# Performance work log

Hardware: AMD Instinct MI355X
Metric: run time of the kernel (lower is better)

## Reference

```python
import jax, jax.numpy as jnp
import numpy as np

D_MODEL, EXPAND, D_STATE, D_CONV, HEADDIM = 1024, 2, 64, 4, 64
D_INNER = EXPAND * D_MODEL          # 2048
NHEADS = D_INNER // HEADDIM         # 32
CONV_DIM = D_INNER + 2 * D_STATE    # x, B, C go through the depthwise conv
D_IN_PROJ = 2 * D_INNER + 2 * D_STATE + NHEADS  # z, xBC, dt
EPS = 1e-5


def setup_inputs() -> dict:
    key = jax.random.key(0)
    ks = jax.random.split(key, 16)
    s = 0.02
    inp = {
        "x": jax.random.normal(ks[0], (2, 2048, D_MODEL), jnp.float32),
        "ln1_w": jnp.ones((D_MODEL,), jnp.float32),
        "ln1_b": jnp.zeros((D_MODEL,), jnp.float32),
        "in_proj_w": jax.random.normal(ks[1], (D_IN_PROJ, D_MODEL), jnp.float32) * s,
        "conv_w": jax.random.normal(ks[2], (CONV_DIM, D_CONV), jnp.float32) * 0.3,
        "conv_b": jnp.zeros((CONV_DIM,), jnp.float32),
        # dt_bias so that softplus(dt+dt_bias) lands in ~[1e-3, 0.1] (mamba2 init)
        "dt_bias": jnp.log(jnp.expm1(jnp.exp(jax.random.uniform(ks[3], (NHEADS,), jnp.float32, jnp.log(1e-3), jnp.log(0.1))))),
        "A_log": jnp.log(jax.random.uniform(ks[4], (NHEADS,), jnp.float32, 1.0, 16.0)),
        "D": jnp.ones((NHEADS,), jnp.float32),
        "norm_w": jnp.ones((D_INNER,), jnp.float32),
        "out_proj_w": jax.random.normal(ks[5], (D_MODEL, D_INNER), jnp.float32) * s,
        "ln2_w": jnp.ones((D_MODEL,), jnp.float32),
        "ln2_b": jnp.zeros((D_MODEL,), jnp.float32),
        "mlp_w1": jax.random.normal(ks[6], (4 * D_MODEL, D_MODEL), jnp.float32) * s,
        "mlp_b1": jnp.zeros((4 * D_MODEL,), jnp.float32),
        "mlp_w2": jax.random.normal(ks[7], (D_MODEL, 4 * D_MODEL), jnp.float32) * s,
        "mlp_b2": jnp.zeros((D_MODEL,), jnp.float32),
    }
    return inp


def _layernorm(x, w, b):
    mu = jnp.mean(x, axis=-1, keepdims=True)
    var = jnp.mean(jnp.square(x - mu), axis=-1, keepdims=True)
    return (x - mu) * jax.lax.rsqrt(var + EPS) * w + b


def _mamba2(x, in_proj_w, conv_w, conv_b, dt_bias, A_log, D, norm_w, out_proj_w):
    Bt, L, _ = x.shape
    zxbcdt = x @ in_proj_w.T                                  # [B,L,D_IN_PROJ]
    z = zxbcdt[..., :D_INNER]
    xBC = zxbcdt[..., D_INNER:D_INNER + CONV_DIM]
    dt = jax.nn.softplus(zxbcdt[..., D_INNER + CONV_DIM:] + dt_bias)  # [B,L,H]
    # causal depthwise conv1d, kernel D_CONV, then SiLU
    xp = jnp.pad(xBC, ((0, 0), (D_CONV - 1, 0), (0, 0)))
    conv = conv_b
    for k in range(D_CONV):
        conv = conv + xp[:, k:k + L, :] * conv_w[:, k]
    xBC = jax.nn.silu(conv)
    xs = xBC[..., :D_INNER].reshape(Bt, L, NHEADS, HEADDIM)   # [B,L,H,P]
    Bm = xBC[..., D_INNER:D_INNER + D_STATE]                  # [B,L,N] (ngroups=1)
    Cm = xBC[..., D_INNER + D_STATE:]                         # [B,L,N]
    A = -jnp.exp(A_log)                                       # [H]

    def step(h, inp):
        x_t, dt_t, B_t, C_t = inp                             # [B,H,P],[B,H],[B,N],[B,N]
        dA = jnp.exp(dt_t * A)                                # [B,H]
        h = h * dA[:, :, None, None] + (dt_t[:, :, None] * x_t)[..., None] * B_t[:, None, None, :]
        y = jnp.einsum('bhpn,bn->bhp', h, C_t)
        return h, y

    h0 = jnp.zeros((Bt, NHEADS, HEADDIM, D_STATE), x.dtype)
    xsT = jnp.moveaxis(xs, 1, 0)
    dtT = jnp.moveaxis(dt, 1, 0)
    BT = jnp.moveaxis(Bm, 1, 0)
    CT = jnp.moveaxis(Cm, 1, 0)
    _, ys = jax.lax.scan(step, h0, (xsT, dtT, BT, CT))        # ys: [L,B,H,P]
    y = jnp.moveaxis(ys, 0, 1) + xs * D[None, None, :, None]  # skip D
    y = y.reshape(Bt, L, D_INNER)
    # gated RMSNorm: rmsnorm(y * silu(z)) * norm_w
    y = y * jax.nn.silu(z)
    y = y * jax.lax.rsqrt(jnp.mean(jnp.square(y), axis=-1, keepdims=True) + EPS) * norm_w
    return y @ out_proj_w.T


def reference(x, ln1_w, ln1_b, in_proj_w, conv_w, conv_b, dt_bias, A_log, D,
              norm_w, out_proj_w, ln2_w, ln2_b, mlp_w1, mlp_b1, mlp_w2, mlp_b2):
    res = x
    h = _layernorm(x, ln1_w, ln1_b)
    h = _mamba2(h, in_proj_w, conv_w, conv_b, dt_bias, A_log, D, norm_w, out_proj_w)
    x = res + h
    res = x
    h = _layernorm(x, ln2_w, ln2_b)
    h = jax.nn.gelu(h @ mlp_w1.T + mlp_b1, approximate=False) @ mlp_w2.T + mlp_b2
    return res + h
```

## Files before the change

kernel.cpp:

```cpp
#include <hip/hip_runtime.h>
#include <hip/hip_bf16.h>
#include <math.h>

using bf16 = __hip_bfloat16;
typedef __attribute__((ext_vector_type(8))) short short8;
typedef __attribute__((ext_vector_type(4))) float floatx4;

#define SEQLEN   2048
#define ROWS     4096
#define DMODEL   1024
#define DINNER   2048
#define NHEADS   32
#define HEADDIM  64
#define DSTATE   64
#define CONVDIM  2176
#define DINPROJ  4256
#define NCHUNK   32

__device__ __forceinline__ float b2f(bf16 x) { return __bfloat162float(x); }
__device__ __forceinline__ bf16  f2b(float x) { return __float2bfloat16(x); }
__device__ __forceinline__ float s2f(short s) { union { short s; bf16 b; } u; u.s = s; return b2f(u.b); }
__device__ __forceinline__ short f2s(float f) { union { short s; bf16 b; } u; u.b = f2b(f); return u.s; }
__device__ __forceinline__ float tof(float x) { return x; }
__device__ __forceinline__ float tof(bf16 x)  { return __bfloat162float(x); }

typedef __attribute__((address_space(1))) void v_as1;
typedef __attribute__((address_space(3))) void v_as3;
__device__ __forceinline__ void gload_lds16(const void* g, void* l) {
  __builtin_amdgcn_global_load_lds((v_as1*)(g), (v_as3*)(l), 16, 0, 0);
}

__global__ void cvt_kernel(const float* __restrict__ in, bf16* __restrict__ out, int n4) {
  int i = blockIdx.x * 256 + threadIdx.x;
  if (i < n4) {
    float4 v = ((const float4*)in)[i];
    union { bf16 h[4]; uint2 u; } r;
    r.h[0] = f2b(v.x); r.h[1] = f2b(v.y); r.h[2] = f2b(v.z); r.h[3] = f2b(v.w);
    ((uint2*)out)[i] = r.u;
  }
}

__device__ __forceinline__ void block_reduce_2(float& a, float& b) {
#pragma unroll
  for (int off = 32; off > 0; off >>= 1) {
    a += __shfl_xor(a, off);
    b += __shfl_xor(b, off);
  }
  __shared__ float ra[4], rb[4];
  int w = threadIdx.x >> 6;
  if ((threadIdx.x & 63) == 0) { ra[w] = a; rb[w] = b; }
  __syncthreads();
  a = ra[0] + ra[1] + ra[2] + ra[3];
  b = rb[0] + rb[1] + rb[2] + rb[3];
}

template<typename TIN>
__global__ void ln_kernel(const TIN* __restrict__ x, const float* __restrict__ w,
                          const float* __restrict__ b, bf16* __restrict__ out)
{
  int row = blockIdx.x;
  int tid = threadIdx.x;
  float v[4]; float s = 0.f, sq = 0.f;
#pragma unroll
  for (int k = 0; k < 4; ++k) {
    int c = k * 256 + tid;
    float xv = tof(x[(size_t)row * DMODEL + c]);
    v[k] = xv; s += xv; sq += xv * xv;
  }
  block_reduce_2(s, sq);
  float mu  = s * (1.f / DMODEL);
  float var = sq * (1.f / DMODEL) - mu * mu;
  float rs  = rsqrtf(var + 1e-5f);
#pragma unroll
  for (int k = 0; k < 4; ++k) {
    int c = k * 256 + tid;
    out[(size_t)row * DMODEL + c] = f2b((v[k] - mu) * rs * w[c] + b[c]);
  }
}

template<int EPI>
__device__ __forceinline__ void epi_store(float v, size_t off, int col,
                                          const float* bias, const void* resid, void* Cout)
{
  if (EPI == 0) {
    ((bf16*)Cout)[off] = f2b(v);
  } else if (EPI == 1) {
    v += bias[col];
    v = 0.5f * v * (1.f + erff(v * 0.70710678118654752f));
    ((bf16*)Cout)[off] = f2b(v);
  } else if (EPI == 2) {
    v += ((const float*)resid)[off];
    ((bf16*)Cout)[off] = f2b(v);
  } else {
    v += bias[col] + b2f(((const bf16*)resid)[off]);
    ((float*)Cout)[off] = v;
  }
}


template<int EPI>
__global__ __launch_bounds__(256, 2)
void gemm_bt(const bf16* __restrict__ A, const bf16* __restrict__ W,
             const float* __restrict__ bias, const void* __restrict__ resid,
             void* __restrict__ Cout, int M, int N, int K)
{
  __shared__ __align__(16) short Asl[128 * 64];
  __shared__ __align__(16) short Bsl[128 * 64];
  const int tid  = threadIdx.x;
  const int lane = tid & 63;
  const int wv   = tid >> 6;
  const int wm   = wv >> 1, wn = wv & 1;
  const int r16  = lane & 15, q = lane >> 4;
  const int m0   = blockIdx.x * 128;
  const int n0   = blockIdx.y * 128;

  floatx4 acc[4][4] = {};

  for (int k0 = 0; k0 < K; k0 += 64) {
#pragma unroll
    for (int it = 0; it < 4; ++it) {
      int idx = it * 256 + tid;
      int row = m0 + (idx >> 3);
      int cb  = (((idx & 7) ^ ((idx >> 3) & 7)) << 3);
      gload_lds16(A + (size_t)row * K + k0 + cb, &Asl[idx * 8]);
    }
#pragma unroll
    for (int it = 0; it < 4; ++it) {
      int idx = it * 256 + tid;
      int row = n0 + (idx >> 3);
      if (row > N - 1) row = N - 1;
      int cb  = (((idx & 7) ^ ((idx >> 3) & 7)) << 3);
      gload_lds16(W + (size_t)row * K + k0 + cb, &Bsl[idx * 8]);
    }
    __syncthreads();
#pragma unroll
    for (int kk = 0; kk < 64; kk += 32) {
      short8 af[4], bfr[4];
      const int lb = (kk >> 3) + q;
#pragma unroll
      for (int i = 0; i < 4; ++i) {
        int ar = wm * 64 + i * 16 + r16;
        af[i] = *(const short8*)&Asl[ar * 64 + ((lb ^ (ar & 7)) << 3)];
      }
#pragma unroll
      for (int j = 0; j < 4; ++j) {
        int br = wn * 64 + j * 16 + r16;
        bfr[j] = *(const short8*)&Bsl[br * 64 + ((lb ^ (br & 7)) << 3)];
      }
#pragma unroll
      for (int i = 0; i < 4; ++i)
#pragma unroll
        for (int j = 0; j < 4; ++j)
          acc[i][j] = __builtin_amdgcn_mfma_f32_16x16x32_bf16(af[i], bfr[j], acc[i][j], 0, 0, 0);
    }
    __syncthreads();
  }

#pragma unroll
  for (int i = 0; i < 4; ++i)
#pragma unroll
    for (int j = 0; j < 4; ++j)
#pragma unroll
      for (int r = 0; r < 4; ++r) {
        int row = m0 + wm * 64 + i * 16 + q * 4 + r;
        int col = n0 + wn * 64 + j * 16 + r16;
        if (col < N)
          epi_store<EPI>(acc[i][j][r], (size_t)row * N + col, col, bias, resid, Cout);
      }
}

template<int EPI>
__global__ __launch_bounds__(256, 4)
void gemm_bt_6464(const bf16* __restrict__ A, const bf16* __restrict__ W,
                  const float* __restrict__ bias, const void* __restrict__ resid,
                  void* __restrict__ Cout, int M, int N, int K)
{
  __shared__ __align__(16) short Asl[64 * 64];
  __shared__ __align__(16) short Bsl[64 * 64];
  const int tid  = threadIdx.x;
  const int lane = tid & 63;
  const int wv   = tid >> 6;
  const int wm   = wv >> 1, wn = wv & 1;
  const int r16  = lane & 15, q = lane >> 4;
  const int m0   = blockIdx.x * 64;
  const int n0   = blockIdx.y * 64;

  floatx4 acc[2][2] = {};

  for (int k0 = 0; k0 < K; k0 += 64) {
#pragma unroll
    for (int it = 0; it < 2; ++it) {
      int idx = it * 256 + tid;
      int cb  = (((idx & 7) ^ ((idx >> 3) & 7)) << 3);
      gload_lds16(A + (size_t)(m0 + (idx >> 3)) * K + k0 + cb, &Asl[idx * 8]);
    }
#pragma unroll
    for (int it = 0; it < 2; ++it) {
      int idx = it * 256 + tid;
      int cb  = (((idx & 7) ^ ((idx >> 3) & 7)) << 3);
      gload_lds16(W + (size_t)(n0 + (idx >> 3)) * K + k0 + cb, &Bsl[idx * 8]);
    }
    __syncthreads();
#pragma unroll
    for (int kk = 0; kk < 64; kk += 32) {
      short8 af[2], bfr[2];
      const int lb = (kk >> 3) + q;
#pragma unroll
      for (int i = 0; i < 2; ++i) {
        int ar = wm * 32 + i * 16 + r16;
        af[i] = *(const short8*)&Asl[ar * 64 + ((lb ^ (ar & 7)) << 3)];
      }
#pragma unroll
      for (int j = 0; j < 2; ++j) {
        int br = wn * 32 + j * 16 + r16;
        bfr[j] = *(const short8*)&Bsl[br * 64 + ((lb ^ (br & 7)) << 3)];
      }
#pragma unroll
      for (int i = 0; i < 2; ++i)
#pragma unroll
        for (int j = 0; j < 2; ++j)
          acc[i][j] = __builtin_amdgcn_mfma_f32_16x16x32_bf16(af[i], bfr[j], acc[i][j], 0, 0, 0);
    }
    __syncthreads();
  }

#pragma unroll
  for (int i = 0; i < 2; ++i)
#pragma unroll
    for (int j = 0; j < 2; ++j)
#pragma unroll
      for (int r = 0; r < 4; ++r) {
        int row = m0 + wm * 32 + i * 16 + q * 4 + r;
        int col = n0 + wn * 32 + j * 16 + r16;
        epi_store<EPI>(acc[i][j][r], (size_t)row * N + col, col, bias, resid, Cout);
      }
}

__global__ void conv_kernel(const bf16* __restrict__ zx, const float* __restrict__ cw,
                            const float* __restrict__ cb, const float* __restrict__ dtbias,
                            bf16* __restrict__ xbc, bf16* __restrict__ Bb,
                            bf16* __restrict__ Cbb, float* __restrict__ dtb)
{
  int row = blockIdx.x;
  int b = row >> 11, t = row & 2047;
  for (int c = threadIdx.x; c < CONVDIM; c += 256) {
    float acc = cb[c];
#pragma unroll
    for (int k = 0; k < 4; ++k) {
      int tt = t + k - 3;
      if (tt >= 0)
        acc += b2f(zx[((size_t)(b * SEQLEN + tt)) * DINPROJ + DINNER + c]) * cw[c * 4 + k];
    }
    float s = acc / (1.f + __expf(-acc));
    xbc[(size_t)row * CONVDIM + c] = f2b(s);
    if (c >= DINNER) {
      if (c < DINNER + DSTATE) Bb[row * DSTATE + (c - DINNER)] = f2b(s);
      else                     Cbb[row * DSTATE + (c - DINNER - DSTATE)] = f2b(s);
    }
  }
  if (threadIdx.x < NHEADS) {
    int hh = threadIdx.x;
    float raw = b2f(zx[(size_t)row * DINPROJ + DINNER + CONVDIM + hh]) + dtbias[hh];
    float dt = raw > 20.f ? raw : log1pf(__expf(raw));
    dtb[row * NHEADS + hh] = dt;
  }
}

__device__ __forceinline__ float wave_incl_prefix(float a, int lane) {
#pragma unroll
  for (int off = 1; off < 64; off <<= 1) {
    float o = __shfl_up(a, off);
    if (lane >= off) a += o;
  }
  return a;
}

__global__ __launch_bounds__(64)
void chunk_state_kernel(const bf16* __restrict__ xbc, const bf16* __restrict__ Bb,
                        const float* __restrict__ dtb, const float* __restrict__ A_log,
                        float* __restrict__ Sbuf, float* __restrict__ Pbuf)
{
  const int blk = blockIdx.x;
  const int c = blk & 31, h = (blk >> 5) & 31, b = blk >> 10;
  const int bh = b * 32 + h;
  const int lane = threadIdx.x;
  const int row = b * SEQLEN + c * 64 + lane;
  const float Ah = -__expf(A_log[h]);

  float dts = dtb[row * NHEADS + h];
  float E = wave_incl_prefix(dts * Ah, lane);
  float EQ = __shfl(E, 63);
  float w = __expf(EQ - E) * dts;
  if (lane == 63) Pbuf[bh * NCHUNK + c] = __expf(EQ);

  __shared__ __align__(16) short XwT[64 * 72];
  __shared__ __align__(16) short BT[64 * 72];

  const bf16* xrow = xbc + (size_t)row * CONVDIM + h * 64;
  const bf16* brow = Bb + (size_t)row * DSTATE;
#pragma unroll
  for (int i = 0; i < 8; ++i) {
    short8 xv = *(const short8*)(xrow + i * 8);
    short8 bv = *(const short8*)(brow + i * 8);
#pragma unroll
    for (int j = 0; j < 8; ++j) {
      XwT[(i * 8 + j) * 72 + lane] = f2s(w * s2f(xv[j]));
      BT[(i * 8 + j) * 72 + lane]  = bv[j];
    }
  }
  __syncthreads();

  const int r16 = lane & 15, q = lane >> 4;
  floatx4 acc[4][4] = {};
#pragma unroll
  for (int kk = 0; kk < 64; kk += 32) {
    short8 af[4], bfr[4];
#pragma unroll
    for (int i = 0; i < 4; ++i) af[i]  = *(const short8*)&XwT[(i * 16 + r16) * 72 + kk + q * 8];
#pragma unroll
    for (int j = 0; j < 4; ++j) bfr[j] = *(const short8*)&BT[(j * 16 + r16) * 72 + kk + q * 8];
#pragma unroll
    for (int i = 0; i < 4; ++i)
#pragma unroll
      for (int j = 0; j < 4; ++j)
        acc[i][j] = __builtin_amdgcn_mfma_f32_16x16x32_bf16(af[i], bfr[j], acc[i][j], 0, 0, 0);
  }
  float* Sout = Sbuf + (size_t)(bh * NCHUNK + c) * 4096;
#pragma unroll
  for (int i = 0; i < 4; ++i)
#pragma unroll
    for (int j = 0; j < 4; ++j)
#pragma unroll
      for (int r = 0; r < 4; ++r)
        Sout[(i * 16 + q * 4 + r) * 64 + (j * 16 + r16)] = acc[i][j][r];
}

__global__ __launch_bounds__(64)
void combine_kernel(const float* __restrict__ Sbuf, const float* __restrict__ Pbuf,
                    bf16* __restrict__ HinB)
{
  const int bh = blockIdx.x >> 2, slab = blockIdx.x & 3;
  const int base = slab * 1024 + threadIdx.x * 16;
  float h[16];
#pragma unroll
  for (int k = 0; k < 16; ++k) h[k] = 0.f;
  for (int c = 0; c < NCHUNK; ++c) {
    size_t off = (size_t)(bh * NCHUNK + c) * 4096 + base;
    union { short s[16]; uint4 q[2]; } pk;
#pragma unroll
    for (int k = 0; k < 16; ++k) pk.s[k] = f2s(h[k]);
    *(uint4*)(HinB + off)     = pk.q[0];
    *(uint4*)(HinB + off + 8) = pk.q[1];
    float P = Pbuf[bh * NCHUNK + c];
    const float4* S4 = (const float4*)(Sbuf + off);
#pragma unroll
    for (int k = 0; k < 4; ++k) {
      float4 s = S4[k];
      h[k*4+0] = h[k*4+0] * P + s.x;
      h[k*4+1] = h[k*4+1] * P + s.y;
      h[k*4+2] = h[k*4+2] * P + s.z;
      h[k*4+3] = h[k*4+3] * P + s.w;
    }
  }
}

__global__ __launch_bounds__(64)
void y_kernel(const bf16* __restrict__ xbc, const bf16* __restrict__ Bb,
              const bf16* __restrict__ Cbb, const float* __restrict__ dtb,
              const bf16* __restrict__ HinB, const float* __restrict__ A_log,
              const float* __restrict__ Dp, bf16* __restrict__ yout)
{
  const int blk = blockIdx.x;
  const int c = blk & 31, h = (blk >> 5) & 31, b = blk >> 10;
  const int bh = b * 32 + h;
  const int lane = threadIdx.x;
  const int row0 = b * SEQLEN + c * 64;
  const int row = row0 + lane;
  const float Ah = -__expf(A_log[h]);
  const float Dh = Dp[h];

  __shared__ __align__(16) short XdT[64 * 72];
  __shared__ __align__(16) short Msh[64 * 72];
  __shared__ float Esh[64];

  float dts = dtb[row * NHEADS + h];
  float E = wave_incl_prefix(dts * Ah, lane);
  Esh[lane] = E;

  const bf16* xrow = xbc + (size_t)row * CONVDIM + h * 64;
#pragma unroll
  for (int i = 0; i < 8; ++i) {
    short8 xv = *(const short8*)(xrow + i * 8);
#pragma unroll
    for (int j = 0; j < 8; ++j)
      XdT[(i * 8 + j) * 72 + lane] = f2s(dts * s2f(xv[j]));
  }
  __syncthreads();

  const int r16 = lane & 15, q = lane >> 4;

  floatx4 accg[4][4] = {};
#pragma unroll
  for (int kk = 0; kk < 64; kk += 32) {
    short8 af[4], bfr[4];
#pragma unroll
    for (int i = 0; i < 4; ++i)
      af[i]  = *(const short8*)(Cbb + (size_t)(row0 + i * 16 + r16) * DSTATE + kk + q * 8);
#pragma unroll
    for (int j = 0; j < 4; ++j)
      bfr[j] = *(const short8*)(Bb + (size_t)(row0 + j * 16 + r16) * DSTATE + kk + q * 8);
#pragma unroll
    for (int i = 0; i < 4; ++i)
#pragma unroll
      for (int j = 0; j < 4; ++j)
        accg[i][j] = __builtin_amdgcn_mfma_f32_16x16x32_bf16(af[i], bfr[j], accg[i][j], 0, 0, 0);
  }
#pragma unroll
  for (int i = 0; i < 4; ++i)
#pragma unroll
    for (int j = 0; j < 4; ++j)
#pragma unroll
      for (int r = 0; r < 4; ++r) {
        int t = i * 16 + q * 4 + r;
        int s = j * 16 + r16;
        float v = (s <= t) ? __expf(Esh[t] - Esh[s]) * accg[i][j][r] : 0.f;
        Msh[t * 72 + s] = f2s(v);
      }
  __syncthreads();

  floatx4 acc[4][4] = {};
#pragma unroll
  for (int kk = 0; kk < 64; kk += 32) {
    short8 af[4], bfr[4];
#pragma unroll
    for (int i = 0; i < 4; ++i) af[i]  = *(const short8*)&Msh[(i * 16 + r16) * 72 + kk + q * 8];
#pragma unroll
    for (int j = 0; j < 4; ++j) bfr[j] = *(const short8*)&XdT[(j * 16 + r16) * 72 + kk + q * 8];
#pragma unroll
    for (int i = 0; i < 4; ++i)
#pragma unroll
      for (int j = 0; j < 4; ++j)
        acc[i][j] = __builtin_amdgcn_mfma_f32_16x16x32_bf16(af[i], bfr[j], acc[i][j], 0, 0, 0);
  }
  float ei[4];
#pragma unroll
  for (int i = 0; i < 4; ++i) ei[i] = __expf(Esh[i * 16 + r16]);
  const bf16* hinp = HinB + (size_t)(bh * NCHUNK + c) * 4096;
#pragma unroll
  for (int kk = 0; kk < 64; kk += 32) {
    short8 af[4], bfr[4];
#pragma unroll
    for (int i = 0; i < 4; ++i) {
      short8 cv = *(const short8*)(Cbb + (size_t)(row0 + i * 16 + r16) * DSTATE + kk + q * 8);
#pragma unroll
      for (int jj = 0; jj < 8; ++jj) af[i][jj] = f2s(ei[i] * s2f(cv[jj]));
    }
#pragma unroll
    for (int j = 0; j < 4; ++j)
      bfr[j] = *(const short8*)(hinp + (j * 16 + r16) * 64 + kk + q * 8);
#pragma unroll
    for (int i = 0; i < 4; ++i)
#pragma unroll
      for (int j = 0; j < 4; ++j)
        acc[i][j] = __builtin_amdgcn_mfma_f32_16x16x32_bf16(af[i], bfr[j], acc[i][j], 0, 0, 0);
  }
#pragma unroll
  for (int i = 0; i < 4; ++i)
#pragma unroll
    for (int j = 0; j < 4; ++j)
#pragma unroll
      for (int r = 0; r < 4; ++r) {
        int t = i * 16 + q * 4 + r;
        int p = j * 16 + r16;
        int g = row0 + t;
        float y = acc[i][j][r] + Dh * b2f(xbc[(size_t)g * CONVDIM + h * 64 + p]);
        yout[(size_t)g * DINNER + h * 64 + p] = f2b(y);
      }
}

__global__ void gate_rms_kernel(const bf16* __restrict__ y, const bf16* __restrict__ zx,
                                const float* __restrict__ nw, bf16* __restrict__ yn)
{
  int row = blockIdx.x, tid = threadIdx.x;
  float v[8]; float ss = 0.f, dummy = 0.f;
#pragma unroll
  for (int k = 0; k < 8; ++k) {
    int c = k * 256 + tid;
    float z = b2f(zx[(size_t)row * DINPROJ + c]);
    float g = z / (1.f + __expf(-z));
    float val = b2f(y[(size_t)row * DINNER + c]) * g;
    v[k] = val; ss += val * val;
  }
  block_reduce_2(ss, dummy);
  float rs = rsqrtf(ss * (1.f / DINNER) + 1e-5f);
#pragma unroll
  for (int k = 0; k < 8; ++k) {
    int c = k * 256 + tid;
    yn[(size_t)row * DINNER + c] = f2b(v[k] * rs * nw[c]);
  }
}

extern "C" void kernel_launch(void* const* d_in, const int* in_sizes, int n_in,
                              void* d_out, int out_size, void* d_ws, size_t ws_size,
                              hipStream_t stream)
{
  const float* x         = (const float*)d_in[0];
  const float* ln1_w     = (const float*)d_in[1];
  const float* ln1_b     = (const float*)d_in[2];
  const float* in_proj_w = (const float*)d_in[3];
  const float* conv_w    = (const float*)d_in[4];
  const float* conv_b    = (const float*)d_in[5];
  const float* dt_bias   = (const float*)d_in[6];
  const float* A_log     = (const float*)d_in[7];
  const float* Dp        = (const float*)d_in[8];
  const float* norm_w    = (const float*)d_in[9];
  const float* out_proj_w= (const float*)d_in[10];
  const float* ln2_w     = (const float*)d_in[11];
  const float* ln2_b     = (const float*)d_in[12];
  const float* mlp_w1    = (const float*)d_in[13];
  const float* mlp_b1    = (const float*)d_in[14];
  const float* mlp_w2    = (const float*)d_in[15];
  const float* mlp_b2    = (const float*)d_in[16];

  char* ws = (char*)d_ws;
  bf16*  zx   = (bf16*)(ws + 0);
  bf16*  h1   = (bf16*)(ws + 34865152);
  bf16*  xbc  = (bf16*)(ws + 43253760);
  bf16*  Bb   = (bf16*)(ws + 61079552);
  bf16*  Cbb  = (bf16*)(ws + 61603840);
  float* dtb  = (float*)(ws + 62128128);
  float* Pbuf = (float*)(ws + 62652416);
  float* Sbuf = (float*)(ws + 62660608);
  bf16*  yw   = (bf16*)(ws + 62660608);
  bf16*  x2   = (bf16*)(ws + 79437824);
  bf16*  HinB = (bf16*)(ws + 96215040);
  bf16*  yn   = (bf16*)(ws + 96215040);
  bf16*  wip  = (bf16*)(ws + 112992256);
  bf16*  wop  = (bf16*)(ws + 121708544);
  bf16*  h2n  = h1;
  bf16*  mid  = zx;
  bf16*  w1b  = wip;
  bf16*  w2b  = xbc;

  cvt_kernel<<<(4256 * 1024 / 4 + 255) / 256, 256, 0, stream>>>(in_proj_w, wip, 4256 * 1024 / 4);
  ln_kernel<float><<<ROWS, 256, 0, stream>>>(x, ln1_w, ln1_b, h1);
  gemm_bt<0><<<dim3(32, 34), 256, 0, stream>>>(h1, wip, nullptr, nullptr, zx,
                                               ROWS, DINPROJ, DMODEL);
  cvt_kernel<<<(4096 * 1024 / 4 + 255) / 256, 256, 0, stream>>>(mlp_w1, w1b, 4096 * 1024 / 4);
  cvt_kernel<<<(1024 * 2048 / 4 + 255) / 256, 256, 0, stream>>>(out_proj_w, wop, 1024 * 2048 / 4);
  conv_kernel<<<ROWS, 256, 0, stream>>>(zx, conv_w, conv_b, dt_bias, xbc, Bb, Cbb, dtb);
  chunk_state_kernel<<<2048, 64, 0, stream>>>(xbc, Bb, dtb, A_log, Sbuf, Pbuf);
  combine_kernel<<<256, 64, 0, stream>>>(Sbuf, Pbuf, HinB);
  y_kernel<<<2048, 64, 0, stream>>>(xbc, Bb, Cbb, dtb, HinB, A_log, Dp, yw);
  cvt_kernel<<<(1024 * 4096 / 4 + 255) / 256, 256, 0, stream>>>(mlp_w2, w2b, 1024 * 4096 / 4);
  gate_rms_kernel<<<ROWS, 256, 0, stream>>>(yw, zx, norm_w, yn);
  gemm_bt_6464<2><<<dim3(64, 16), 256, 0, stream>>>(yn, wop, nullptr, x, (void*)x2,
                                                    ROWS, DMODEL, DINNER);
  ln_kernel<bf16><<<ROWS, 256, 0, stream>>>(x2, ln2_w, ln2_b, h2n);
  gemm_bt<1><<<dim3(32, 32), 256, 0, stream>>>(h2n, w1b, mlp_b1, nullptr, mid,
                                               ROWS, 4 * DMODEL, DMODEL);
  gemm_bt_6464<3><<<dim3(64, 16), 256, 0, stream>>>(mid, w2b, mlp_b2, x2, d_out,
                                                    ROWS, DMODEL, 4 * DMODEL);
}
```

Baseline: 430.3 us.

## Use intra-block split-K across waves for 64x64 output-projection and MLP-down GEMMs

The 64x64 tile GEMM now loads 128-wide K slabs, and each of the four waves computes the full 64x64 tile over its own 32-wide K slice instead of a 32x32 sub-tile. Partial sums are reduced through shared memory before the epilogue. The goal is fewer barriers per unit of K and more MFMA work per fragment load. In exchange it uses more accumulator registers (64 floats per lane), larger shared memory, and an extra reduction pass with several syncs that may reduce occupancy.

```diff
diff --git a/kernel.cpp b/kernel.cpp
--- a/kernel.cpp
+++ b/kernel.cpp
@@ -171,69 +171,110 @@
 
 template<int EPI>
 __global__ __launch_bounds__(256, 4)
-void gemm_bt_6464(const bf16* __restrict__ A, const bf16* __restrict__ W,
+void gemm_bt_64sk(const bf16* __restrict__ A, const bf16* __restrict__ W,
                   const float* __restrict__ bias, const void* __restrict__ resid,
                   void* __restrict__ Cout, int M, int N, int K)
 {
-  __shared__ __align__(16) short Asl[64 * 64];
-  __shared__ __align__(16) short Bsl[64 * 64];
+  __shared__ __align__(16) char smem[2][64 * 66 * 4];
+  short* Asl  = (short*)smem[0];
+  short* Bsl  = (short*)smem[1];
+  float* red0 = (float*)smem[0];
+  float* red1 = (float*)smem[1];
+
   const int tid  = threadIdx.x;
   const int lane = tid & 63;
   const int wv   = tid >> 6;
-  const int wm   = wv >> 1, wn = wv & 1;
   const int r16  = lane & 15, q = lane >> 4;
   const int m0   = blockIdx.x * 64;
   const int n0   = blockIdx.y * 64;
 
-  floatx4 acc[2][2] = {};
-
-  for (int k0 = 0; k0 < K; k0 += 64) {
-#pragma unroll
-    for (int it = 0; it < 2; ++it) {
+  floatx4 acc[4][4] = {};
+
+  for (int k0 = 0; k0 < K; k0 += 128) {
+#pragma unroll
+    for (int it = 0; it < 4; ++it) {
       int idx = it * 256 + tid;
-      int cb  = (((idx & 7) ^ ((idx >> 3) & 7)) << 3);
-      gload_lds16(A + (size_t)(m0 + (idx >> 3)) * K + k0 + cb, &Asl[idx * 8]);
-    }
-#pragma unroll
-    for (int it = 0; it < 2; ++it) {
+      int row = idx >> 4;
+      int cb  = (((idx & 15) ^ (row & 15)) << 3);
+      gload_lds16(A + (size_t)(m0 + row) * K + k0 + cb, &Asl[idx * 8]);
+    }
+#pragma unroll
+    for (int it = 0; it < 4; ++it) {
       int idx = it * 256 + tid;
-      int cb  = (((idx & 7) ^ ((idx >> 3) & 7)) << 3);
-      gload_lds16(W + (size_t)(n0 + (idx >> 3)) * K + k0 + cb, &Bsl[idx * 8]);
+      int row = idx >> 4;
+      int cb  = (((idx & 15) ^ (row & 15)) << 3);
+      gload_lds16(W + (size_t)(n0 + row) * K + k0 + cb, &Bsl[idx * 8]);
     }
     __syncthreads();
-#pragma unroll
-    for (int kk = 0; kk < 64; kk += 32) {
-      short8 af[2], bfr[2];
-      const int lb = (kk >> 3) + q;
-#pragma unroll
-      for (int i = 0; i < 2; ++i) {
-        int ar = wm * 32 + i * 16 + r16;
-        af[i] = *(const short8*)&Asl[ar * 64 + ((lb ^ (ar & 7)) << 3)];
+    {
+      short8 af[4], bfr[4];
+      const int lb = wv * 4 + q;
+#pragma unroll
+      for (int i = 0; i < 4; ++i) {
+        int ar = i * 16 + r16;
+        af[i] = *(const short8*)&Asl[ar * 128 + ((lb ^ (ar & 15)) << 3)];
       }
 #pragma unroll
-      for (int j = 0; j < 2; ++j) {
-        int br = wn * 32 + j * 16 + r16;
-        bfr[j] = *(const short8*)&Bsl[br * 64 + ((lb ^ (br & 7)) << 3)];
+      for (int j = 0; j < 4; ++j) {
+        int br = j * 16 + r16;
+        bfr[j] = *(const short8*)&Bsl[br * 128 + ((lb ^ (br & 15)) << 3)];
       }
 #pragma unroll
-      for (int i = 0; i < 2; ++i)
-#pragma unroll
-        for (int j = 0; j < 2; ++j)
+      for (int i = 0; i < 4; ++i)
+#pragma unroll
+        for (int j = 0; j < 4; ++j)
           acc[i][j] = __builtin_amdgcn_mfma_f32_16x16x32_bf16(af[i], bfr[j], acc[i][j], 0, 0, 0);
     }
     __syncthreads();
   }
 
-#pragma unroll
-  for (int i = 0; i < 2; ++i)
-#pragma unroll
-    for (int j = 0; j < 2; ++j)
-#pragma unroll
-      for (int r = 0; r < 4; ++r) {
-        int row = m0 + wm * 32 + i * 16 + q * 4 + r;
-        int col = n0 + wn * 32 + j * 16 + r16;
-        epi_store<EPI>(acc[i][j][r], (size_t)row * N + col, col, bias, resid, Cout);
-      }
+  if (wv >= 2) {
+    float* dst = (wv == 2) ? red0 : red1;
+#pragma unroll
+    for (int i = 0; i < 4; ++i)
+#pragma unroll
+      for (int j = 0; j < 4; ++j)
+#pragma unroll
+        for (int r = 0; r < 4; ++r)
+          dst[(i * 16 + q * 4 + r) * 66 + j * 16 + r16] = acc[i][j][r];
+  }
+  __syncthreads();
+  if (wv < 2) {
+    float* src = (wv == 0) ? red0 : red1;
+#pragma unroll
+    for (int i = 0; i < 4; ++i)
+#pragma unroll
+      for (int j = 0; j < 4; ++j)
+#pragma unroll
+        for (int r = 0; r < 4; ++r)
+          acc[i][j][r] += src[(i * 16 + q * 4 + r) * 66 + j * 16 + r16];
+  }
+  __syncthreads();
+  if (wv == 0) {
+#pragma unroll
+    for (int i = 0; i < 4; ++i)
+#pragma unroll
+      for (int j = 0; j < 4; ++j)
+#pragma unroll
+        for (int r = 0; r < 4; ++r)
+          red0[(i * 16 + q * 4 + r) * 66 + j * 16 + r16] = acc[i][j][r];
+  } else if (wv == 1) {
+#pragma unroll
+    for (int i = 0; i < 4; ++i)
+#pragma unroll
+      for (int j = 0; j < 4; ++j)
+#pragma unroll
+        for (int r = 0; r < 4; ++r)
+          red1[(i * 16 + q * 4 + r) * 66 + j * 16 + r16] = acc[i][j][r];
+  }
+  __syncthreads();
+#pragma unroll
+  for (int k = 0; k < 16; ++k) {
+    int e   = tid * 16 + k;
+    int row = e >> 6, col = e & 63;
+    float v = red0[row * 66 + col] + red1[row * 66 + col];
+    epi_store<EPI>(v, (size_t)(m0 + row) * N + (n0 + col), n0 + col, bias, resid, Cout);
+  }
 }
 
 __global__ void conv_kernel(const bf16* __restrict__ zx, const float* __restrict__ cw,
@@ -554,11 +595,11 @@
   y_kernel<<<2048, 64, 0, stream>>>(xbc, Bb, Cbb, dtb, HinB, A_log, Dp, yw);
   cvt_kernel<<<(1024 * 4096 / 4 + 255) / 256, 256, 0, stream>>>(mlp_w2, w2b, 1024 * 4096 / 4);
   gate_rms_kernel<<<ROWS, 256, 0, stream>>>(yw, zx, norm_w, yn);
-  gemm_bt_6464<2><<<dim3(64, 16), 256, 0, stream>>>(yn, wop, nullptr, x, (void*)x2,
+  gemm_bt_64sk<2><<<dim3(64, 16), 256, 0, stream>>>(yn, wop, nullptr, x, (void*)x2,
                                                     ROWS, DMODEL, DINNER);
   ln_kernel<bf16><<<ROWS, 256, 0, stream>>>(x2, ln2_w, ln2_b, h2n);
   gemm_bt<1><<<dim3(32, 32), 256, 0, stream>>>(h2n, w1b, mlp_b1, nullptr, mid,
                                                ROWS, 4 * DMODEL, DMODEL);
-  gemm_bt_6464<3><<<dim3(64, 16), 256, 0, stream>>>(mid, w2b, mlp_b2, x2, d_out,
+  gemm_bt_64sk<3><<<dim3(64, 16), 256, 0, stream>>>(mid, w2b, mlp_b2, x2, d_out,
                                                     ROWS, DMODEL, 4 * DMODEL);
 }
```

Measured after the change: 439.1 us. 2.0% more time.

## Double-buffer LDS tiles in both GEMM kernels to overlap loads with MFMA

Applied to the files above, without the earlier changes.

Both bf16 GEMM kernels now keep two LDS buffers per operand and issue the global-to-LDS loads for the next K tile before computing on the current one. Partial vmcnt waits plus raw barriers replace the two __syncthreads per iteration, so memory latency can hide behind MFMA work. The cost is twice the LDS per block (64KB for the 128x128 kernel), which can lower occupancy below the launch_bounds target of 2 blocks per CU. The hand-written waitcnt counts depend on exactly how many loads each stage issues.

```diff
diff --git a/kernel.cpp b/kernel.cpp
--- a/kernel.cpp
+++ b/kernel.cpp
@@ -104,8 +104,8 @@
              const float* __restrict__ bias, const void* __restrict__ resid,
              void* __restrict__ Cout, int M, int N, int K)
 {
-  __shared__ __align__(16) short Asl[128 * 64];
-  __shared__ __align__(16) short Bsl[128 * 64];
+  __shared__ __align__(16) short Asl[2][128 * 64];
+  __shared__ __align__(16) short Bsl[2][128 * 64];
   const int tid  = threadIdx.x;
   const int lane = tid & 63;
   const int wv   = tid >> 6;
@@ -116,13 +116,13 @@
 
   floatx4 acc[4][4] = {};
 
-  for (int k0 = 0; k0 < K; k0 += 64) {
+  auto stage = [&](int b, int k0) {
 #pragma unroll
     for (int it = 0; it < 4; ++it) {
       int idx = it * 256 + tid;
       int row = m0 + (idx >> 3);
       int cb  = (((idx & 7) ^ ((idx >> 3) & 7)) << 3);
-      gload_lds16(A + (size_t)row * K + k0 + cb, &Asl[idx * 8]);
+      gload_lds16(A + (size_t)row * K + k0 + cb, &Asl[b][idx * 8]);
     }
 #pragma unroll
     for (int it = 0; it < 4; ++it) {
@@ -130,9 +130,10 @@
       int row = n0 + (idx >> 3);
       if (row > N - 1) row = N - 1;
       int cb  = (((idx & 7) ^ ((idx >> 3) & 7)) << 3);
-      gload_lds16(W + (size_t)row * K + k0 + cb, &Bsl[idx * 8]);
-    }
-    __syncthreads();
+      gload_lds16(W + (size_t)row * K + k0 + cb, &Bsl[b][idx * 8]);
+    }
+  };
+  auto compute = [&](int b) {
 #pragma unroll
     for (int kk = 0; kk < 64; kk += 32) {
       short8 af[4], bfr[4];
@@ -140,12 +141,12 @@
 #pragma unroll
       for (int i = 0; i < 4; ++i) {
         int ar = wm * 64 + i * 16 + r16;
-        af[i] = *(const short8*)&Asl[ar * 64 + ((lb ^ (ar & 7)) << 3)];
+        af[i] = *(const short8*)&Asl[b][ar * 64 + ((lb ^ (ar & 7)) << 3)];
       }
 #pragma unroll
       for (int j = 0; j < 4; ++j) {
         int br = wn * 64 + j * 16 + r16;
-        bfr[j] = *(const short8*)&Bsl[br * 64 + ((lb ^ (br & 7)) << 3)];
+        bfr[j] = *(const short8*)&Bsl[b][br * 64 + ((lb ^ (br & 7)) << 3)];
       }
 #pragma unroll
       for (int i = 0; i < 4; ++i)
@@ -153,8 +154,23 @@
         for (int j = 0; j < 4; ++j)
           acc[i][j] = __builtin_amdgcn_mfma_f32_16x16x32_bf16(af[i], bfr[j], acc[i][j], 0, 0, 0);
     }
-    __syncthreads();
-  }
+  };
+
+  stage(0, 0);
+  const int nt = K >> 6;
+  int cur = 0;
+  for (int t = 0; t < nt - 1; ++t) {
+    stage(cur ^ 1, (t + 1) << 6);
+    asm volatile("s_waitcnt vmcnt(8)" ::: "memory");
+    __builtin_amdgcn_s_barrier();
+    compute(cur);
+    asm volatile("s_waitcnt lgkmcnt(0)" ::: "memory");
+    __builtin_amdgcn_s_barrier();
+    cur ^= 1;
+  }
+  asm volatile("s_waitcnt vmcnt(0)" ::: "memory");
+  __builtin_amdgcn_s_barrier();
+  compute(cur);
 
 #pragma unroll
   for (int i = 0; i < 4; ++i)
@@ -175,8 +191,8 @@
                   const float* __restrict__ bias, const void* __restrict__ resid,
                   void* __restrict__ Cout, int M, int N, int K)
 {
-  __shared__ __align__(16) short Asl[64 * 64];
-  __shared__ __align__(16) short Bsl[64 * 64];
+  __shared__ __align__(16) short Asl[2][64 * 64];
+  __shared__ __align__(16) short Bsl[2][64 * 64];
   const int tid  = threadIdx.x;
   const int lane = tid & 63;
   const int wv   = tid >> 6;
@@ -187,20 +203,21 @@
 
   floatx4 acc[2][2] = {};
 
-  for (int k0 = 0; k0 < K; k0 += 64) {
+  auto stage = [&](int b, int k0) {
 #pragma unroll
     for (int it = 0; it < 2; ++it) {
       int idx = it * 256 + tid;
       int cb  = (((idx & 7) ^ ((idx >> 3) & 7)) << 3);
-      gload_lds16(A + (size_t)(m0 + (idx >> 3)) * K + k0 + cb, &Asl[idx * 8]);
+      gload_lds16(A + (size_t)(m0 + (idx >> 3)) * K + k0 + cb, &Asl[b][idx * 8]);
     }
 #pragma unroll
     for (int it = 0; it < 2; ++it) {
       int idx = it * 256 + tid;
       int cb  = (((idx & 7) ^ ((idx >> 3) & 7)) << 3);
-      gload_lds16(W + (size_t)(n0 + (idx >> 3)) * K + k0 + cb, &Bsl[idx * 8]);
-    }
-    __syncthreads();
+      gload_lds16(W + (size_t)(n0 + (idx >> 3)) * K + k0 + cb, &Bsl[b][idx * 8]);
+    }
+  };
+  auto compute = [&](int b) {
 #pragma unroll
     for (int kk = 0; kk < 64; kk += 32) {
       short8 af[2], bfr[2];
@@ -208,12 +225,12 @@
 #pragma unroll
       for (int i = 0; i < 2; ++i) {
         int ar = wm * 32 + i * 16 + r16;
-        af[i] = *(const short8*)&Asl[ar * 64 + ((lb ^ (ar & 7)) << 3)];
+        af[i] = *(const short8*)&Asl[b][ar * 64 + ((lb ^ (ar & 7)) << 3)];
       }
 #pragma unroll
       for (int j = 0; j < 2; ++j) {
         int br = wn * 32 + j * 16 + r16;
-        bfr[j] = *(const short8*)&Bsl[br * 64 + ((lb ^ (br & 7)) << 3)];
+        bfr[j] = *(const short8*)&Bsl[b][br * 64 + ((lb ^ (br & 7)) << 3)];
       }
 #pragma unroll
       for (int i = 0; i < 2; ++i)
@@ -221,8 +238,23 @@
         for (int j = 0; j < 2; ++j)
           acc[i][j] = __builtin_amdgcn_mfma_f32_16x16x32_bf16(af[i], bfr[j], acc[i][j], 0, 0, 0);
     }
-    __syncthreads();
-  }
+  };
+
+  stage(0, 0);
+  const int nt = K >> 6;
+  int cur = 0;
+  for (int t = 0; t < nt - 1; ++t) {
+    stage(cur ^ 1, (t + 1) << 6);
+    asm volatile("s_waitcnt vmcnt(4)" ::: "memory");
+    __builtin_amdgcn_s_barrier();
+    compute(cur);
+    asm volatile("s_waitcnt lgkmcnt(0)" ::: "memory");
+    __builtin_amdgcn_s_barrier();
+    cur ^= 1;
+  }
+  asm volatile("s_waitcnt vmcnt(0)" ::: "memory");
+  __builtin_amdgcn_s_barrier();
+  compute(cur);
 
 #pragma unroll
   for (int i = 0; i < 2; ++i)
```

Measured after the change: 442.2 us. 1.03x slower.
